# Kernel optimization log

Hardware: AMD Instinct MI355X
Metric: run time of the kernel (lower is better)

## Reference

```python
import jax, jax.numpy as jnp
import numpy as np

B, SEQ, K, H = 4096, 50, 4, 64   # batch, seq_len, interest_num, hidden_size
ROUTING_TIMES = 3


def setup_inputs() -> dict:
    key = jax.random.key(0)
    k1, k2, k3 = jax.random.split(key, 3)
    mask = jax.random.randint(k1, (B, SEQ), 0, 2, dtype=jnp.int32)
    item_eb_hat = jax.random.normal(k2, (B, SEQ, K, H), dtype=jnp.float32)
    capsule_weight = jax.random.normal(k3, (B, K, SEQ), dtype=jnp.float32)
    return {"mask": mask, "item_eb_hat": item_eb_hat, "capsule_weight": capsule_weight}


def _squash(v):
    # v: [B, K, 1, H]
    cap_norm = jnp.sum(jnp.square(v), -1, keepdims=True)
    scalar = cap_norm / (1.0 + cap_norm) / jnp.sqrt(cap_norm + 1e-9)
    return scalar * v


def reference(mask, item_eb_hat, capsule_weight):
    # [B, seq, K, H] -> [B, K, seq, H]
    x = jnp.transpose(item_eb_hat.reshape(-1, SEQ, K, H), (0, 2, 1, 3))
    x_iter = jax.lax.stop_gradient(x)  # stop_grad=True in the module
    # attention mask broadcast to [B, K, seq]
    am = jnp.broadcast_to(mask[:, None, :], capsule_weight.shape)
    interest_capsule = None
    for i in range(ROUTING_TIMES):
        # torch F.softmax without dim on a 3D tensor -> dim=0 (batch axis); faithful.
        w = jax.nn.softmax(capsule_weight, axis=0)
        w = jnp.where(am == 0, jnp.zeros_like(w), w)[:, :, None, :]  # [B,K,1,seq]
        if i < ROUTING_TIMES - 1:
            interest_capsule = _squash(jnp.matmul(w, x_iter))          # [B,K,1,H]
            delta = jnp.matmul(x_iter, jnp.swapaxes(interest_capsule, -1, -2))  # [B,K,seq,1]
            capsule_weight = capsule_weight + delta.reshape(-1, K, SEQ)
        else:
            interest_capsule = _squash(jnp.matmul(w, x))               # [B,K,1,H]
    return interest_capsule.reshape(-1, K, H)
```

## Files before the change

kernel.cpp:

```cpp
#include <hip/hip_runtime.h>
#include <math.h>

#define BB 4096
#define SEQ 50
#define KK 4
#define HH 64
#define NCOL (KK*SEQ)
#define NPART 64
#define BPP (BB/NPART)

__global__ void init_kernel(const float* __restrict__ cw,
                            float* __restrict__ part0,
                            float* __restrict__ part1,
                            float* __restrict__ part2) {
    const int p = blockIdx.x;
    const int t = threadIdx.x;
    if (t < NCOL) {
        const float* row = cw + (size_t)p * BPP * NCOL + t;
        float s = 0.f;
#pragma unroll 8
        for (int b = 0; b < BPP; b++) s += __expf(row[b * NCOL]);
        part0[p * NCOL + t] = s;
        part1[p * NCOL + t] = 0.f;
        part2[p * NCOL + t] = 0.f;
    }
}

template <int ITER>
__global__ void update_kernel(const float* __restrict__ cw_src,
                              float* __restrict__ cw_dst,
                              const float* __restrict__ x,
                              const int* __restrict__ mask,
                              const float* __restrict__ part_in,
                              float* __restrict__ part_out,
                              float* __restrict__ out) {
    const int b = blockIdx.x;
    const int k = threadIdx.x >> 6;
    const int h = threadIdx.x & 63;

    __shared__ float scol[NCOL];

    if (threadIdx.x < NCOL) {
        float s = 0.f;
#pragma unroll 16
        for (int p = 0; p < NPART; p++) s += part_in[p * NCOL + threadIdx.x];
        scol[threadIdx.x] = s;
    }

    const float* xp = x + (size_t)b * (SEQ * KK * HH) + k * HH + h;
    float xrow[SEQ];
#pragma unroll
    for (int s = 0; s < SEQ; s++) xrow[s] = xp[s * (KK * HH)];

    __syncthreads();

    float wlane = 0.f, c = 0.f;
    if (h < SEQ) {
        c = cw_src[(size_t)b * NCOL + k * SEQ + h];
        float e = __expf(c) / scol[k * SEQ + h];
        wlane = (mask[b * SEQ + h] != 0) ? e : 0.f;
    }

    float v = 0.f;
#pragma unroll
    for (int s = 0; s < SEQ; s++) v = fmaf(__shfl(wlane, s, 64), xrow[s], v);

    float n2 = v * v;
#pragma unroll
    for (int off = 32; off >= 1; off >>= 1) n2 += __shfl_xor(n2, off, 64);
    const float scalar = n2 / ((1.f + n2) * sqrtf(n2 + 1e-9f));
    v *= scalar;

    if (ITER == 2) {
        out[(size_t)b * (KK * HH) + k * HH + h] = v;
    } else {
        float myd = 0.f;
#pragma unroll
        for (int s = 0; s < SEQ; s++) {
            float p = xrow[s] * v;
#pragma unroll
            for (int off = 32; off >= 1; off >>= 1) p += __shfl_xor(p, off, 64);
            if (s == h) myd = p;
        }
        if (h < SEQ) {
            const float nc = c + myd;
            cw_dst[(size_t)b * NCOL + k * SEQ + h] = nc;
            atomicAdd(&part_out[(b >> 6) * NCOL + k * SEQ + h], __expf(nc));
        }
    }
}

extern "C" void kernel_launch(void* const* d_in, const int* in_sizes, int n_in,
                              void* d_out, int out_size, void* d_ws, size_t ws_size,
                              hipStream_t stream) {
    const int*   mask  = (const int*)d_in[0];
    const float* x     = (const float*)d_in[1];
    const float* cw_in = (const float*)d_in[2];
    float* out = (float*)d_out;

    float* cw_ws = (float*)d_ws;
    float* part0 = cw_ws + (size_t)BB * NCOL;
    float* part1 = part0 + NPART * NCOL;
    float* part2 = part1 + NPART * NCOL;

    init_kernel<<<NPART, 256, 0, stream>>>(cw_in, part0, part1, part2);
    update_kernel<0><<<BB, 256, 0, stream>>>(cw_in, cw_ws, x, mask, part0, part1, nullptr);
    update_kernel<1><<<BB, 256, 0, stream>>>(cw_ws, cw_ws, x, mask, part1, part2, nullptr);
    update_kernel<2><<<BB, 256, 0, stream>>>(cw_ws, nullptr, x, mask, part2, nullptr, out);
}
```

Before: 401.5 us.

## Replace shuffle reductions with readlane broadcasts and per-lane transposed dot products

The weighted sum now broadcasts the softmax weights with readlane instead of ds_bpermute shuffles, and streams x directly from memory instead of caching 50 values per thread in registers. The delta computation used 50 butterfly reductions of 6 shuffles each; each lane now computes its own dot product by reading its x row with float4 loads and broadcasting v with readlane. This removes about 300 cross-lane shuffles per wave and lowers register pressure. In exchange, x is read twice from global memory or cache, with an uncoalesced strided pattern in the second pass.

```diff
diff --git a/kernel.cpp b/kernel.cpp
--- a/kernel.cpp
+++ b/kernel.cpp
@@ -8,6 +8,10 @@
 #define NCOL (KK*SEQ)
 #define NPART 64
 #define BPP (BB/NPART)
+
+__device__ __forceinline__ float readlane_f32(float v, int lane) {
+    return __int_as_float(__builtin_amdgcn_readlane(__float_as_int(v), lane));
+}
 
 __global__ void init_kernel(const float* __restrict__ cw,
                             float* __restrict__ part0,
@@ -37,6 +41,7 @@
     const int b = blockIdx.x;
     const int k = threadIdx.x >> 6;
     const int h = threadIdx.x & 63;
+    const int hs = (h < SEQ) ? h : 0;
 
     __shared__ float scol[NCOL];
 
@@ -47,23 +52,19 @@
         scol[threadIdx.x] = s;
     }
 
-    const float* xp = x + (size_t)b * (SEQ * KK * HH) + k * HH + h;
-    float xrow[SEQ];
-#pragma unroll
-    for (int s = 0; s < SEQ; s++) xrow[s] = xp[s * (KK * HH)];
+    const float c = cw_src[(size_t)b * NCOL + k * SEQ + hs];
+    const int  mk = mask[b * SEQ + hs];
 
     __syncthreads();
 
-    float wlane = 0.f, c = 0.f;
-    if (h < SEQ) {
-        c = cw_src[(size_t)b * NCOL + k * SEQ + h];
-        float e = __expf(c) / scol[k * SEQ + h];
-        wlane = (mask[b * SEQ + h] != 0) ? e : 0.f;
-    }
+    const float e = __expf(c) / scol[k * SEQ + hs];
+    const float wlane = (h < SEQ && mk != 0) ? e : 0.f;
 
+    const float* xp = x + (size_t)b * (SEQ * KK * HH) + k * HH + h;
     float v = 0.f;
 #pragma unroll
-    for (int s = 0; s < SEQ; s++) v = fmaf(__shfl(wlane, s, 64), xrow[s], v);
+    for (int s = 0; s < SEQ; s++)
+        v = fmaf(readlane_f32(wlane, s), xp[s * (KK * HH)], v);
 
     float n2 = v * v;
 #pragma unroll
@@ -74,16 +75,28 @@
     if (ITER == 2) {
         out[(size_t)b * (KK * HH) + k * HH + h] = v;
     } else {
-        float myd = 0.f;
+        const float* xt = x + (size_t)b * (SEQ * KK * HH) + hs * (KK * HH) + k * HH;
+        float g[16];
 #pragma unroll
-        for (int s = 0; s < SEQ; s++) {
-            float p = xrow[s] * v;
+        for (int j4 = 0; j4 < 16; j4++) {
+            const float4 xv = *(const float4*)(xt + j4 * 4);
+            const float p0 = xv.x * readlane_f32(v, 4 * j4 + 0);
+            const float p1 = xv.y * readlane_f32(v, 4 * j4 + 1);
+            const float p2 = xv.z * readlane_f32(v, 4 * j4 + 2);
+            const float p3 = xv.w * readlane_f32(v, 4 * j4 + 3);
+            g[j4] = (p0 + p1) + (p2 + p3);
+        }
+        float t8[8], t4[4], t2[2];
 #pragma unroll
-            for (int off = 32; off >= 1; off >>= 1) p += __shfl_xor(p, off, 64);
-            if (s == h) myd = p;
-        }
+        for (int i = 0; i < 8; i++) t8[i] = g[2 * i] + g[2 * i + 1];
+#pragma unroll
+        for (int i = 0; i < 4; i++) t4[i] = t8[2 * i] + t8[2 * i + 1];
+#pragma unroll
+        for (int i = 0; i < 2; i++) t2[i] = t4[2 * i] + t4[2 * i + 1];
+        const float del = t2[0] + t2[1];
+
         if (h < SEQ) {
-            const float nc = c + myd;
+            const float nc = c + del;
             cw_dst[(size_t)b * NCOL + k * SEQ + h] = nc;
             atomicAdd(&part_out[(b >> 6) * NCOL + k * SEQ + h], __expf(nc));
         }
```

After: 389.4 us. 3.0% less time.
